# Kernel optimization log

Measured on AMD Instinct MI355X. Metric: run time of the kernel, lower is better.

## Reference

```python
import jax, jax.numpy as jnp
import numpy as np
import math

B, S, H = 8, 160, 768
DEP = 64
NH, DH = 12, H // 12
W_EDGE = 1.0
EPS = 1e-5


def setup_inputs() -> dict:
    key = jax.random.key(0)
    ks = jax.random.split(key, 16)
    sc_h = 1.0 / math.sqrt(H)
    sc_d = 1.0 / math.sqrt(DEP)
    return {
        "token_feature": jax.random.normal(ks[0], (B, S, H), jnp.float32),
        "edge_feature": jax.random.normal(ks[1], (B, S, S, DEP), jnp.float32),
        "dependency_masks": jax.random.randint(ks[2], (B, S, S), 0, 2, jnp.int32),
        "Wq": jax.random.normal(ks[3], (H, H), jnp.float32) * sc_h,
        "bq": jnp.zeros((H,), jnp.float32),
        "Wk": jax.random.normal(ks[4], (H, H), jnp.float32) * sc_h,
        "bk": jnp.zeros((H,), jnp.float32),
        "Wv": jax.random.normal(ks[5], (H, H), jnp.float32) * sc_h,
        "bv": jnp.zeros((H,), jnp.float32),
        "Wek": jax.random.normal(ks[6], (DEP, H), jnp.float32) * sc_d,
        "bek": jnp.zeros((H,), jnp.float32),
        "Wev": jax.random.normal(ks[7], (DEP, H), jnp.float32) * sc_d,
        "bev": jnp.zeros((H,), jnp.float32),
        "ln_g": jnp.ones((H,), jnp.float32),
        "ln_b": jnp.zeros((H,), jnp.float32),
    }


def _heads3(x):  # [B,S,H] -> [B,NH,S,DH]
    return x.reshape(B, S, NH, DH).transpose(0, 2, 1, 3)


def _heads4(x):  # [B,S,S,H] -> [B,NH,S,S,DH]
    return x.reshape(B, S, S, NH, DH).transpose(0, 3, 1, 2, 4)


def reference(token_feature, edge_feature, dependency_masks,
              Wq, bq, Wk, bk, Wv, bv, Wek, bek, Wev, bev, ln_g, ln_b):
    q = _heads3(token_feature @ Wq + bq)   # [B,NH,S,DH]
    k = _heads3(token_feature @ Wk + bk)
    v = _heads3(token_feature @ Wv + bv)
    ek = _heads4(edge_feature @ Wek + bek)  # [B,NH,S,S,DH]
    ev = _heads4(edge_feature @ Wev + bev)
    # key_ij = k_j + w*ek_ij ; scores_ij = q_i . key_ij / sqrt(dh)
    scores = (jnp.einsum('bhid,bhjd->bhij', q, k)
              + W_EDGE * jnp.einsum('bhid,bhijd->bhij', q, ek))
    scores = scores / math.sqrt(DH)
    mask = (dependency_masks[:, None, :, :] == 0)  # [B,1,S,S]
    scores = jnp.where(mask, jnp.float32(-10000.0), scores)
    probs = jax.nn.softmax(scores, axis=-1)  # dropout is identity in eval
    ctx = (jnp.einsum('bhij,bhjd->bhid', probs, v)
           + W_EDGE * jnp.einsum('bhij,bhijd->bhid', probs, ev))
    ctx = ctx.transpose(0, 2, 1, 3).reshape(B, S, H)
    x = token_feature + ctx
    mu = jnp.mean(x, axis=-1, keepdims=True)
    var = jnp.mean(jnp.square(x - mu), axis=-1, keepdims=True)
    return (x - mu) / jnp.sqrt(var + EPS) * ln_g + ln_b
```

## Files before the change

### kernel.cpp

```cpp
#include <hip/hip_runtime.h>
#include <hip/hip_bf16.h>
#include <math.h>

#define BB 8
#define SS 160
#define HH 768
#define DEPTH 64
#define NHEAD 12
#define DHEAD 64
#define BS (BB*SS)
#define SCROW (NHEAD*SS)

constexpr float EPS_C = 1e-5f;

typedef __attribute__((ext_vector_type(8))) short bf16x8;
typedef __attribute__((ext_vector_type(4))) float f32x4;

__device__ inline short f2bs(float x) {
    union { __hip_bfloat16 b; short s; } u;
    u.b = __float2bfloat16(x);
    return u.s;
}

__global__ __launch_bounds__(256) void transpose_cast_w(
    const float* __restrict__ Wq, const float* __restrict__ Wk,
    const float* __restrict__ Wv, __hip_bfloat16* __restrict__ WT)
{
    __shared__ float t[32][33];
    const float* W = (blockIdx.z == 0) ? Wq : (blockIdx.z == 1) ? Wk : Wv;
    __hip_bfloat16* o = WT + (size_t)blockIdx.z * HH * HH;
    int kt = blockIdx.x * 32, nt = blockIdx.y * 32;
    int tx = threadIdx.x & 31, ty = threadIdx.x >> 5;
#pragma unroll
    for (int r = 0; r < 32; r += 8)
        t[ty + r][tx] = W[(size_t)(kt + ty + r) * HH + nt + tx];
    __syncthreads();
#pragma unroll
    for (int r = 0; r < 32; r += 8)
        o[(size_t)(nt + ty + r) * HH + kt + tx] = __float2bfloat16(t[tx][ty + r]);
}

__global__ __launch_bounds__(256) void gemm_qkv(
    const float* __restrict__ X, const __hip_bfloat16* __restrict__ WT,
    const float* __restrict__ bq, const float* __restrict__ bk,
    const float* __restrict__ bv,
    __hip_bfloat16* __restrict__ qb, __hip_bfloat16* __restrict__ kb,
    __hip_bfloat16* __restrict__ vb)
{
    __shared__ int4 sA[4][128];
    __shared__ int4 sB[4][64];
    int m0 = blockIdx.x * 128, n0 = blockIdx.y * 64, mat = blockIdx.z;
    const short* W = (const short*)WT + (size_t)mat * HH * HH;
    const float* bias = (mat == 0) ? bq : (mat == 1) ? bk : bv;
    int tid = threadIdx.x, w = tid >> 6, l = tid & 63;
    int wm = (w >> 1) * 64, wn = (w & 1) * 32;
    int khalf = l >> 4, lc = l & 15;

    f32x4 acc[4][2];
#pragma unroll
    for (int i = 0; i < 4; i++)
#pragma unroll
        for (int j = 0; j < 2; j++) acc[i][j] = (f32x4){0.f, 0.f, 0.f, 0.f};

    for (int k0 = 0; k0 < HH; k0 += 32) {
        __syncthreads();
#pragma unroll
        for (int rr = 0; rr < 2; rr++) {
            const float* ap = X + (size_t)(m0 + l + rr * 64) * HH + k0 + w * 8;
            float4 x0 = *(const float4*)ap;
            float4 x1 = *(const float4*)(ap + 4);
            bf16x8 p;
            p[0]=f2bs(x0.x); p[1]=f2bs(x0.y); p[2]=f2bs(x0.z); p[3]=f2bs(x0.w);
            p[4]=f2bs(x1.x); p[5]=f2bs(x1.y); p[6]=f2bs(x1.z); p[7]=f2bs(x1.w);
            *(bf16x8*)&sA[w][l + rr * 64] = p;
        }
        sB[w][l] = *(const int4*)(W + (size_t)(n0 + l) * HH + k0 + w * 8);
        __syncthreads();
        bf16x8 b0 = *(const bf16x8*)&sB[khalf][wn + lc];
        bf16x8 b1 = *(const bf16x8*)&sB[khalf][wn + 16 + lc];
#pragma unroll
        for (int mi = 0; mi < 4; mi++) {
            bf16x8 a = *(const bf16x8*)&sA[khalf][wm + mi * 16 + lc];
            acc[mi][0] = __builtin_amdgcn_mfma_f32_16x16x32_bf16(a, b0, acc[mi][0], 0, 0, 0);
            acc[mi][1] = __builtin_amdgcn_mfma_f32_16x16x32_bf16(a, b1, acc[mi][1], 0, 0, 0);
        }
    }

    int rg = (l >> 4) * 4;
    __hip_bfloat16* outm = (mat == 0) ? qb : (mat == 1) ? kb : vb;
#pragma unroll
    for (int ni = 0; ni < 2; ni++) {
        int gcol = n0 + wn + ni * 16 + lc;
        float bv_ = bias[gcol];
#pragma unroll
        for (int mi = 0; mi < 4; mi++) {
            int grow = m0 + wm + mi * 16 + rg;
            f32x4 a = acc[mi][ni];
            __hip_bfloat16* o = outm + (size_t)grow * HH + gcol;
            o[0]      = __float2bfloat16(a.x + bv_);
            o[HH]     = __float2bfloat16(a.y + bv_);
            o[2 * HH] = __float2bfloat16(a.z + bv_);
            o[3 * HH] = __float2bfloat16(a.w + bv_);
        }
    }
}

__global__ __launch_bounds__(256) void scores_gemm(
    const __hip_bfloat16* __restrict__ qb, const __hip_bfloat16* __restrict__ kb,
    _Float16* __restrict__ sc)
{
    __shared__ int4 sQ[8][160];
    __shared__ int4 sK[8][160];
    int h = blockIdx.x, b = blockIdx.y;
    const short* Q = (const short*)qb + (size_t)b * SS * HH + h * DHEAD;
    const short* K = (const short*)kb + (size_t)b * SS * HH + h * DHEAD;
    int tid = threadIdx.x, w = tid >> 6, l = tid & 63;

    for (int idx = tid; idx < SS * 8; idx += 256) {
        int row = idx >> 3, ch = idx & 7;
        sQ[ch][row] = *(const int4*)(Q + (size_t)row * HH + ch * 8);
        sK[ch][row] = *(const int4*)(K + (size_t)row * HH + ch * 8);
    }
    __syncthreads();

    int wm = (w >> 1) * 80, wn = (w & 1) * 80;
    int khalf = l >> 4, lc = l & 15;
    f32x4 acc[5][5];
#pragma unroll
    for (int i = 0; i < 5; i++)
#pragma unroll
        for (int j = 0; j < 5; j++) acc[i][j] = (f32x4){0.f, 0.f, 0.f, 0.f};

#pragma unroll
    for (int s = 0; s < 2; s++) {
        int c = s * 4 + khalf;
        bf16x8 bf[5];
#pragma unroll
        for (int ni = 0; ni < 5; ni++)
            bf[ni] = *(const bf16x8*)&sK[c][wn + ni * 16 + lc];
#pragma unroll
        for (int mi = 0; mi < 5; mi++) {
            bf16x8 a = *(const bf16x8*)&sQ[c][wm + mi * 16 + lc];
#pragma unroll
            for (int ni = 0; ni < 5; ni++)
                acc[mi][ni] = __builtin_amdgcn_mfma_f32_16x16x32_bf16(a, bf[ni], acc[mi][ni], 0, 0, 0);
        }
    }

    int rg = (l >> 4) * 4;
    _Float16* base = sc + ((size_t)b * SS) * SCROW + (size_t)h * SS;
#pragma unroll
    for (int mi = 0; mi < 5; mi++) {
        int i0 = wm + mi * 16 + rg;
#pragma unroll
        for (int ni = 0; ni < 5; ni++) {
            int j = wn + ni * 16 + lc;
            f32x4 a = acc[mi][ni];
            base[(size_t)(i0 + 0) * SCROW + j] = (_Float16)(a.x * 0.125f);
            base[(size_t)(i0 + 1) * SCROW + j] = (_Float16)(a.y * 0.125f);
            base[(size_t)(i0 + 2) * SCROW + j] = (_Float16)(a.z * 0.125f);
            base[(size_t)(i0 + 3) * SCROW + j] = (_Float16)(a.w * 0.125f);
        }
    }
}

__global__ __launch_bounds__(256) void qek_slim(
    const __hip_bfloat16* __restrict__ qb, const float* __restrict__ Wek,
    __hip_bfloat16* __restrict__ qek)
{
    __shared__ short sW[8 * 65 * 8];
    int h = blockIdx.x, mg = blockIdx.y;
    int tid = threadIdx.x, w = tid >> 6, l = tid & 63;
    int lr = l & 15, kg = l >> 4;

    {
        int d = tid >> 2, q4 = tid & 3;
        const float* wp = Wek + (size_t)d * HH + h * DHEAD + q4 * 16;
        float4 w0 = *(const float4*)(wp);
        float4 w1 = *(const float4*)(wp + 4);
        float4 w2 = *(const float4*)(wp + 8);
        float4 w3 = *(const float4*)(wp + 12);
        bf16x8 p0, p1;
        p0[0]=f2bs(w0.x); p0[1]=f2bs(w0.y); p0[2]=f2bs(w0.z); p0[3]=f2bs(w0.w);
        p0[4]=f2bs(w1.x); p0[5]=f2bs(w1.y); p0[6]=f2bs(w1.z); p0[7]=f2bs(w1.w);
        p1[0]=f2bs(w2.x); p1[1]=f2bs(w2.y); p1[2]=f2bs(w2.z); p1[3]=f2bs(w2.w);
        p1[4]=f2bs(w3.x); p1[5]=f2bs(w3.y); p1[6]=f2bs(w3.z); p1[7]=f2bs(w3.w);
        *(bf16x8*)&sW[((q4 * 2) * 65 + d) * 8]     = p0;
        *(bf16x8*)&sW[((q4 * 2 + 1) * 65 + d) * 8] = p1;
    }
    __syncthreads();

    bf16x8 bfrag[2][4];
#pragma unroll
    for (int s = 0; s < 2; s++)
#pragma unroll
        for (int nt = 0; nt < 4; nt++)
            bfrag[s][nt] = *(const bf16x8*)&sW[((s * 4 + kg) * 65 + nt * 16 + lr) * 8];

    const short* Q = (const short*)qb;
    short* O = (short*)qek;
    int m0 = (mg * 4 + w) * 16;
    bf16x8 a0 = *(const bf16x8*)(Q + (size_t)(m0 + lr) * HH + h * DHEAD + kg * 8);
    bf16x8 a1 = *(const bf16x8*)(Q + (size_t)(m0 + lr) * HH + h * DHEAD + 32 + kg * 8);
#pragma unroll
    for (int nt = 0; nt < 4; nt++) {
        f32x4 acc = (f32x4){0.f, 0.f, 0.f, 0.f};
        acc = __builtin_amdgcn_mfma_f32_16x16x32_bf16(a0, bfrag[0][nt], acc, 0, 0, 0);
        acc = __builtin_amdgcn_mfma_f32_16x16x32_bf16(a1, bfrag[1][nt], acc, 0, 0, 0);
        int row0 = m0 + kg * 4;
#pragma unroll
        for (int r = 0; r < 4; r++)
            O[(size_t)(row0 + r) * HH + h * DHEAD + nt * 16 + lr] = f2bs(acc[r]);
    }
}

__global__ __launch_bounds__(256) void attn_kernel(
    const float* __restrict__ token, const float* __restrict__ edge,
    const int* __restrict__ mask,
    const __hip_bfloat16* __restrict__ q_ws, const _Float16* __restrict__ sc,
    const __hip_bfloat16* __restrict__ v_ws, const __hip_bfloat16* __restrict__ qek,
    const float* __restrict__ bek,
    const float* __restrict__ Wev, const float* __restrict__ bev,
    const float* __restrict__ ln_g, const float* __restrict__ ln_b,
    float* __restrict__ out)
{
    __shared__ float  s_ctx[HH];
    __shared__ float  s_scores[NHEAD][SS + 2];
    __shared__ float  s_pe[NHEAD][DEPTH];
    __shared__ float  s_x[HH];
    __shared__ float  s_qbek[NHEAD];
    __shared__ int    s_mask[SS];
    __shared__ float  s_red[8];

    int bi = blockIdx.x;
    int b  = bi / SS;
    int tid = threadIdx.x;
    int w = tid >> 6, l = tid & 63;
    int lr = l & 15, kg = l >> 4;

    if (tid < SS) s_mask[tid] = mask[(size_t)bi * SS + tid];

    {
        int hs = w * 3 + kg;
        float part = 0.f;
        if (hs < NHEAD) {
            const __hip_bfloat16* qp = q_ws + (size_t)bi * HH + hs * DHEAD + lr * 4;
            float4 bv4 = *(const float4*)(bek + hs * DHEAD + lr * 4);
            part = __bfloat162float(qp[0]) * bv4.x + __bfloat162float(qp[1]) * bv4.y
                 + __bfloat162float(qp[2]) * bv4.z + __bfloat162float(qp[3]) * bv4.w;
        }
        part += __shfl_xor(part, 1, 64);
        part += __shfl_xor(part, 2, 64);
        part += __shfl_xor(part, 4, 64);
        part += __shfl_xor(part, 8, 64);
        if (lr == 0 && hs < NHEAD) s_qbek[hs] = part;
    }
    __syncthreads();

    const float* scf = (const float*)(sc + (size_t)bi * SCROW);
    for (int idx = tid; idx < SCROW / 2; idx += 256) {
        int h = idx / (SS / 2), jp = idx - h * (SS / 2);
        union { float f; _Float16 e[2]; } u;
        u.f = scf[idx];
        int j = jp * 2;
        s_scores[h][j]     = s_mask[j]     ? ((float)u.e[0] + 0.125f * s_qbek[h]) : -10000.0f;
        s_scores[h][j + 1] = s_mask[j + 1] ? ((float)u.e[1] + 0.125f * s_qbek[h]) : -10000.0f;
    }
    __syncthreads();

    const float* e_row = edge + (size_t)bi * SS * DEPTH;
    {
        const short* QE = (const short*)qek + (size_t)bi * HH;
        bf16x8 qe0 = *(const bf16x8*)(QE + lr * DHEAD + kg * 8);
        bf16x8 qe1 = *(const bf16x8*)(QE + lr * DHEAD + 32 + kg * 8);
        for (int jt = w; jt < 10; jt += 4) {
            const float* ep = e_row + (size_t)(jt * 16 + lr) * DEPTH + kg * 8;
            float4 e0 = *(const float4*)(ep);
            float4 e1 = *(const float4*)(ep + 4);
            float4 e2 = *(const float4*)(ep + 32);
            float4 e3 = *(const float4*)(ep + 36);
            bf16x8 a0, a1;
            a0[0]=f2bs(e0.x); a0[1]=f2bs(e0.y); a0[2]=f2bs(e0.z); a0[3]=f2bs(e0.w);
            a0[4]=f2bs(e1.x); a0[5]=f2bs(e1.y); a0[6]=f2bs(e1.z); a0[7]=f2bs(e1.w);
            a1[0]=f2bs(e2.x); a1[1]=f2bs(e2.y); a1[2]=f2bs(e2.z); a1[3]=f2bs(e2.w);
            a1[4]=f2bs(e3.x); a1[5]=f2bs(e3.y); a1[6]=f2bs(e3.z); a1[7]=f2bs(e3.w);
            f32x4 acc = (f32x4){0.f, 0.f, 0.f, 0.f};
            acc = __builtin_amdgcn_mfma_f32_16x16x32_bf16(a0, qe0, acc, 0, 0, 0);
            acc = __builtin_amdgcn_mfma_f32_16x16x32_bf16(a1, qe1, acc, 0, 0, 0);
            if (lr < NHEAD) {
                int j0 = jt * 16 + kg * 4;
#pragma unroll
                for (int r = 0; r < 4; r++)
                    if (s_mask[j0 + r])
                        s_scores[lr][j0 + r] += 0.125f * acc[r];
            }
        }
    }
    __syncthreads();

    for (int h = w; h < NHEAD; h += 4) {
        float v0 = s_scores[h][l];
        float v1 = s_scores[h][l + 64];
        float v2 = (l < 32) ? s_scores[h][l + 128] : -INFINITY;
        float mx = fmaxf(v0, fmaxf(v1, v2));
#pragma unroll
        for (int mm = 32; mm >= 1; mm >>= 1) mx = fmaxf(mx, __shfl_xor(mx, mm, 64));
        float e0 = expf(v0 - mx), e1 = expf(v1 - mx);
        float e2 = (l < 32) ? expf(v2 - mx) : 0.f;
        float sm = e0 + e1 + e2;
#pragma unroll
        for (int mm = 32; mm >= 1; mm >>= 1) sm += __shfl_xor(sm, mm, 64);
        float inv = 1.0f / sm;
        s_scores[h][l]      = e0 * inv;
        s_scores[h][l + 64] = e1 * inv;
        if (l < 32) s_scores[h][l + 128] = e2 * inv;
    }
    __syncthreads();

    {
        int h0 = w * 3;
        float av0 = 0.f, av1 = 0.f, av2 = 0.f;
        float pe0 = 0.f, pe1 = 0.f, pe2 = 0.f;
        const __hip_bfloat16* vbp = v_ws + (size_t)b * SS * HH + h0 * DHEAD + l;
        const float* er = e_row + l;
#pragma unroll 2
        for (int j0 = 0; j0 < SS; j0 += 2) {
            float2 p0 = *(const float2*)(&s_scores[h0][j0]);
            float2 p1 = *(const float2*)(&s_scores[h0 + 1][j0]);
            float2 p2 = *(const float2*)(&s_scores[h0 + 2][j0]);
            const __hip_bfloat16* vp = vbp + (size_t)j0 * HH;
            av0 += p0.x * __bfloat162float(vp[0])
                 + p0.y * __bfloat162float(vp[HH]);
            av1 += p1.x * __bfloat162float(vp[DHEAD])
                 + p1.y * __bfloat162float(vp[HH + DHEAD]);
            av2 += p2.x * __bfloat162float(vp[2 * DHEAD])
                 + p2.y * __bfloat162float(vp[HH + 2 * DHEAD]);
            float ev0 = er[(size_t)j0 * DEPTH];
            float ev1 = er[(size_t)(j0 + 1) * DEPTH];
            pe0 += p0.x * ev0 + p0.y * ev1;
            pe1 += p1.x * ev0 + p1.y * ev1;
            pe2 += p2.x * ev0 + p2.y * ev1;
        }
        s_pe[h0][l]     = pe0;
        s_pe[h0 + 1][l] = pe1;
        s_pe[h0 + 2][l] = pe2;
        s_ctx[h0 * DHEAD + l]       = av0;
        s_ctx[(h0 + 1) * DHEAD + l] = av1;
        s_ctx[(h0 + 2) * DHEAD + l] = av2;
    }
    __syncthreads();

    for (int mdx = tid; mdx < HH; mdx += 256) {
        int h = mdx >> 6;
        const float* pep = &s_pe[h][0];
        float sum = 0.f;
#pragma unroll
        for (int d = 0; d < DEPTH; d++) sum += pep[d] * Wev[(size_t)d * HH + mdx];
        float ctx = s_ctx[mdx] + (sum + bev[mdx]);
        s_x[mdx] = token[(size_t)bi * HH + mdx] + ctx;
    }
    __syncthreads();

    float lsum = 0.f, lsq = 0.f;
    for (int c = tid; c < HH; c += 256) {
        float x = s_x[c];
        lsum += x; lsq += x * x;
    }
#pragma unroll
    for (int mm = 32; mm >= 1; mm >>= 1) {
        lsum += __shfl_xor(lsum, mm, 64);
        lsq  += __shfl_xor(lsq,  mm, 64);
    }
    if (l == 0) { s_red[w] = lsum; s_red[4 + w] = lsq; }
    __syncthreads();
    float tsum = s_red[0] + s_red[1] + s_red[2] + s_red[3];
    float tsq  = s_red[4] + s_red[5] + s_red[6] + s_red[7];
    float mu  = tsum / HH;
    float var = tsq / HH - mu * mu;
    float rstd = rsqrtf(var + EPS_C);
    for (int c = tid; c < HH; c += 256)
        out[(size_t)bi * HH + c] = (s_x[c] - mu) * rstd * ln_g[c] + ln_b[c];
}

extern "C" void kernel_launch(void* const* d_in, const int* in_sizes, int n_in,
                              void* d_out, int out_size, void* d_ws, size_t ws_size,
                              hipStream_t stream) {
    const float* token = (const float*)d_in[0];
    const float* edge  = (const float*)d_in[1];
    const int*   mask  = (const int*)d_in[2];
    const float* Wq = (const float*)d_in[3];  const float* bq = (const float*)d_in[4];
    const float* Wk = (const float*)d_in[5];  const float* bk = (const float*)d_in[6];
    const float* Wv = (const float*)d_in[7];  const float* bv = (const float*)d_in[8];
    const float* Wek = (const float*)d_in[9];  const float* bek = (const float*)d_in[10];
    const float* Wev = (const float*)d_in[11]; const float* bev = (const float*)d_in[12];
    const float* ln_g = (const float*)d_in[13]; const float* ln_b = (const float*)d_in[14];
    float* out = (float*)d_out;

    __hip_bfloat16* qb = (__hip_bfloat16*)d_ws;
    __hip_bfloat16* kb = qb + (size_t)BS * HH;
    __hip_bfloat16* vb = kb + (size_t)BS * HH;
    __hip_bfloat16* WT = vb + (size_t)BS * HH;
    _Float16*       sc = (_Float16*)WT;
    __hip_bfloat16* qek = kb;

    transpose_cast_w<<<dim3(24, 24, 3), 256, 0, stream>>>(Wq, Wk, Wv, WT);
    gemm_qkv<<<dim3(BS / 128, HH / 64, 3), 256, 0, stream>>>(
        token, WT, bq, bk, bv, qb, kb, vb);
    scores_gemm<<<dim3(NHEAD, BB), 256, 0, stream>>>(qb, kb, sc);
    qek_slim<<<dim3(NHEAD, 20), 256, 0, stream>>>(qb, Wek, qek);
    attn_kernel<<<BS, 256, 0, stream>>>(token, edge, mask, qb, sc, vb, qek,
                                        bek, Wev, bev, ln_g, ln_b, out);
}
```

Measured before the change: 113.1 us.

## Store V transposed and split edge-score MFMA into a separate kernel

The QKV GEMM now writes V in a per-batch transposed layout so the attention kernel can load eight consecutive keys per lane with one vector load instead of scalar strided bf16 loads. The edge-key score contribution (edge x qek via MFMA) moves out of the attention kernel into a new escore_add2 kernel that adds into the fp16 score buffer in global memory, shortening attn_kernel and removing one barrier. The trade-off is an extra launch, an extra read-modify-write pass over the score buffer with fp16 rounding of the combined score, and strided transposed stores in the GEMM epilogue. The edge tensor is also read twice, once per kernel.

Result: slower. 200.2 us (+77.1%).

```diff
diff --git a/kernel.cpp b/kernel.cpp
--- a/kernel.cpp
+++ b/kernel.cpp
@@ -21,6 +21,11 @@
     u.b = __float2bfloat16(x);
     return u.s;
 }
+__device__ inline float bs2f(short s) {
+    union { short s; __hip_bfloat16 b; } u;
+    u.s = s;
+    return __bfloat162float(u.b);
+}
 
 __global__ __launch_bounds__(256) void transpose_cast_w(
     const float* __restrict__ Wq, const float* __restrict__ Wk,
@@ -45,7 +50,7 @@
     const float* __restrict__ bq, const float* __restrict__ bk,
     const float* __restrict__ bv,
     __hip_bfloat16* __restrict__ qb, __hip_bfloat16* __restrict__ kb,
-    __hip_bfloat16* __restrict__ vb)
+    __hip_bfloat16* __restrict__ vTb)
 {
     __shared__ int4 sA[4][128];
     __shared__ int4 sB[4][64];
@@ -87,7 +92,6 @@
     }
 
     int rg = (l >> 4) * 4;
-    __hip_bfloat16* outm = (mat == 0) ? qb : (mat == 1) ? kb : vb;
 #pragma unroll
     for (int ni = 0; ni < 2; ni++) {
         int gcol = n0 + wn + ni * 16 + lc;
@@ -96,11 +100,20 @@
         for (int mi = 0; mi < 4; mi++) {
             int grow = m0 + wm + mi * 16 + rg;
             f32x4 a = acc[mi][ni];
-            __hip_bfloat16* o = outm + (size_t)grow * HH + gcol;
-            o[0]      = __float2bfloat16(a.x + bv_);
-            o[HH]     = __float2bfloat16(a.y + bv_);
-            o[2 * HH] = __float2bfloat16(a.z + bv_);
-            o[3 * HH] = __float2bfloat16(a.w + bv_);
+            if (mat == 2) {
+                int bb = grow / SS; int i0 = grow - bb * SS;
+                __hip_bfloat16* dst = vTb + ((size_t)bb * HH + gcol) * SS + i0;
+                dst[0] = __float2bfloat16(a.x + bv_);
+                dst[1] = __float2bfloat16(a.y + bv_);
+                dst[2] = __float2bfloat16(a.z + bv_);
+                dst[3] = __float2bfloat16(a.w + bv_);
+            } else {
+                __hip_bfloat16* o = ((mat == 0) ? qb : kb) + (size_t)grow * HH + gcol;
+                o[0]      = __float2bfloat16(a.x + bv_);
+                o[HH]     = __float2bfloat16(a.y + bv_);
+                o[2 * HH] = __float2bfloat16(a.z + bv_);
+                o[3 * HH] = __float2bfloat16(a.w + bv_);
+            }
         }
     }
 }
@@ -214,11 +227,53 @@
     }
 }
 
+__global__ __launch_bounds__(256) void escore_add2(
+    const float* __restrict__ edge, const __hip_bfloat16* __restrict__ qek,
+    _Float16* __restrict__ sc)
+{
+    int task = blockIdx.x * 4 + (threadIdx.x >> 6);
+    int l = threadIdx.x & 63;
+    int bi = task / 5, seg = task - (task / 5) * 5;
+    int lr = l & 15, kg = l >> 4;
+
+    const short* QE = (const short*)qek + (size_t)bi * HH;
+    bf16x8 qe0 = *(const bf16x8*)(QE + lr * DHEAD + kg * 8);
+    bf16x8 qe1 = *(const bf16x8*)(QE + lr * DHEAD + 32 + kg * 8);
+
+    const float* E = edge + (size_t)bi * SS * DEPTH;
+    _Float16* srow = sc + (size_t)bi * SCROW;
+
+#pragma unroll
+    for (int t = 0; t < 2; t++) {
+        int jt = seg * 2 + t;
+        const float* ep = E + (size_t)(jt * 16 + lr) * DEPTH + kg * 8;
+        float4 e0 = *(const float4*)(ep);
+        float4 e1 = *(const float4*)(ep + 4);
+        float4 e2 = *(const float4*)(ep + 32);
+        float4 e3 = *(const float4*)(ep + 36);
+        bf16x8 a0, a1;
+        a0[0]=f2bs(e0.x); a0[1]=f2bs(e0.y); a0[2]=f2bs(e0.z); a0[3]=f2bs(e0.w);
+        a0[4]=f2bs(e1.x); a0[5]=f2bs(e1.y); a0[6]=f2bs(e1.z); a0[7]=f2bs(e1.w);
+        a1[0]=f2bs(e2.x); a1[1]=f2bs(e2.y); a1[2]=f2bs(e2.z); a1[3]=f2bs(e2.w);
+        a1[4]=f2bs(e3.x); a1[5]=f2bs(e3.y); a1[6]=f2bs(e3.z); a1[7]=f2bs(e3.w);
+        f32x4 acc = (f32x4){0.f, 0.f, 0.f, 0.f};
+        acc = __builtin_amdgcn_mfma_f32_16x16x32_bf16(a0, qe0, acc, 0, 0, 0);
+        acc = __builtin_amdgcn_mfma_f32_16x16x32_bf16(a1, qe1, acc, 0, 0, 0);
+        if (lr < NHEAD) {
+            int j0 = jt * 16 + kg * 4;
+            _Float16* p = srow + (size_t)lr * SS + j0;
+#pragma unroll
+            for (int r = 0; r < 4; r++)
+                p[r] = (_Float16)((float)p[r] + 0.125f * acc[r]);
+        }
+    }
+}
+
 __global__ __launch_bounds__(256) void attn_kernel(
     const float* __restrict__ token, const float* __restrict__ edge,
     const int* __restrict__ mask,
     const __hip_bfloat16* __restrict__ q_ws, const _Float16* __restrict__ sc,
-    const __hip_bfloat16* __restrict__ v_ws, const __hip_bfloat16* __restrict__ qek,
+    const __hip_bfloat16* __restrict__ vT,
     const float* __restrict__ bek,
     const float* __restrict__ Wev, const float* __restrict__ bev,
     const float* __restrict__ ln_g, const float* __restrict__ ln_b,
@@ -268,36 +323,6 @@
     }
     __syncthreads();
 
-    const float* e_row = edge + (size_t)bi * SS * DEPTH;
-    {
-        const short* QE = (const short*)qek + (size_t)bi * HH;
-        bf16x8 qe0 = *(const bf16x8*)(QE + lr * DHEAD + kg * 8);
-        bf16x8 qe1 = *(const bf16x8*)(QE + lr * DHEAD + 32 + kg * 8);
-        for (int jt = w; jt < 10; jt += 4) {
-            const float* ep = e_row + (size_t)(jt * 16 + lr) * DEPTH + kg * 8;
-            float4 e0 = *(const float4*)(ep);
-            float4 e1 = *(const float4*)(ep + 4);
-            float4 e2 = *(const float4*)(ep + 32);
-            float4 e3 = *(const float4*)(ep + 36);
-            bf16x8 a0, a1;
-            a0[0]=f2bs(e0.x); a0[1]=f2bs(e0.y); a0[2]=f2bs(e0.z); a0[3]=f2bs(e0.w);
-            a0[4]=f2bs(e1.x); a0[5]=f2bs(e1.y); a0[6]=f2bs(e1.z); a0[7]=f2bs(e1.w);
-            a1[0]=f2bs(e2.x); a1[1]=f2bs(e2.y); a1[2]=f2bs(e2.z); a1[3]=f2bs(e2.w);
-            a1[4]=f2bs(e3.x); a1[5]=f2bs(e3.y); a1[6]=f2bs(e3.z); a1[7]=f2bs(e3.w);
-            f32x4 acc = (f32x4){0.f, 0.f, 0.f, 0.f};
-            acc = __builtin_amdgcn_mfma_f32_16x16x32_bf16(a0, qe0, acc, 0, 0, 0);
-            acc = __builtin_amdgcn_mfma_f32_16x16x32_bf16(a1, qe1, acc, 0, 0, 0);
-            if (lr < NHEAD) {
-                int j0 = jt * 16 + kg * 4;
-#pragma unroll
-                for (int r = 0; r < 4; r++)
-                    if (s_mask[j0 + r])
-                        s_scores[lr][j0 + r] += 0.125f * acc[r];
-            }
-        }
-    }
-    __syncthreads();
-
     for (int h = w; h < NHEAD; h += 4) {
         float v0 = s_scores[h][l];
         float v1 = s_scores[h][l + 64];
@@ -317,29 +342,33 @@
     }
     __syncthreads();
 
+    const float* e_row = edge + (size_t)bi * SS * DEPTH;
     {
         int h0 = w * 3;
         float av0 = 0.f, av1 = 0.f, av2 = 0.f;
         float pe0 = 0.f, pe1 = 0.f, pe2 = 0.f;
-        const __hip_bfloat16* vbp = v_ws + (size_t)b * SS * HH + h0 * DHEAD + l;
+        const __hip_bfloat16* vt0 = vT + ((size_t)b * HH + h0 * DHEAD + l) * SS;
+        const __hip_bfloat16* vt1 = vt0 + (size_t)DHEAD * SS;
+        const __hip_bfloat16* vt2 = vt1 + (size_t)DHEAD * SS;
         const float* er = e_row + l;
-#pragma unroll 2
-        for (int j0 = 0; j0 < SS; j0 += 2) {
-            float2 p0 = *(const float2*)(&s_scores[h0][j0]);
-            float2 p1 = *(const float2*)(&s_scores[h0 + 1][j0]);
-            float2 p2 = *(const float2*)(&s_scores[h0 + 2][j0]);
-            const __hip_bfloat16* vp = vbp + (size_t)j0 * HH;
-            av0 += p0.x * __bfloat162float(vp[0])
-                 + p0.y * __bfloat162float(vp[HH]);
-            av1 += p1.x * __bfloat162float(vp[DHEAD])
-                 + p1.y * __bfloat162float(vp[HH + DHEAD]);
-            av2 += p2.x * __bfloat162float(vp[2 * DHEAD])
-                 + p2.y * __bfloat162float(vp[HH + 2 * DHEAD]);
-            float ev0 = er[(size_t)j0 * DEPTH];
-            float ev1 = er[(size_t)(j0 + 1) * DEPTH];
-            pe0 += p0.x * ev0 + p0.y * ev1;
-            pe1 += p1.x * ev0 + p1.y * ev1;
-            pe2 += p2.x * ev0 + p2.y * ev1;
+        for (int j0 = 0; j0 < SS; j0 += 8) {
+            bf16x8 v0 = *(const bf16x8*)(vt0 + j0);
+            bf16x8 v1 = *(const bf16x8*)(vt1 + j0);
+            bf16x8 v2 = *(const bf16x8*)(vt2 + j0);
+#pragma unroll
+            for (int r = 0; r < 8; r += 2) {
+                float2 p0 = *(const float2*)(&s_scores[h0][j0 + r]);
+                float2 p1 = *(const float2*)(&s_scores[h0 + 1][j0 + r]);
+                float2 p2 = *(const float2*)(&s_scores[h0 + 2][j0 + r]);
+                float ev0 = er[(size_t)(j0 + r) * DEPTH];
+                float ev1 = er[(size_t)(j0 + r + 1) * DEPTH];
+                av0 += p0.x * bs2f(v0[r]) + p0.y * bs2f(v0[r + 1]);
+                av1 += p1.x * bs2f(v1[r]) + p1.y * bs2f(v1[r + 1]);
+                av2 += p2.x * bs2f(v2[r]) + p2.y * bs2f(v2[r + 1]);
+                pe0 += p0.x * ev0 + p0.y * ev1;
+                pe1 += p1.x * ev0 + p1.y * ev1;
+                pe2 += p2.x * ev0 + p2.y * ev1;
+            }
         }
         s_pe[h0][l]     = pe0;
         s_pe[h0 + 1][l] = pe1;
@@ -398,16 +427,17 @@
 
     __hip_bfloat16* qb = (__hip_bfloat16*)d_ws;
     __hip_bfloat16* kb = qb + (size_t)BS * HH;
-    __hip_bfloat16* vb = kb + (size_t)BS * HH;
-    __hip_bfloat16* WT = vb + (size_t)BS * HH;
+    __hip_bfloat16* vT = kb + (size_t)BS * HH;
+    __hip_bfloat16* WT = vT + (size_t)BS * HH;
     _Float16*       sc = (_Float16*)WT;
     __hip_bfloat16* qek = kb;
 
     transpose_cast_w<<<dim3(24, 24, 3), 256, 0, stream>>>(Wq, Wk, Wv, WT);
     gemm_qkv<<<dim3(BS / 128, HH / 64, 3), 256, 0, stream>>>(
-        token, WT, bq, bk, bv, qb, kb, vb);
+        token, WT, bq, bk, bv, qb, kb, vT);
     scores_gemm<<<dim3(NHEAD, BB), 256, 0, stream>>>(qb, kb, sc);
     qek_slim<<<dim3(NHEAD, 20), 256, 0, stream>>>(qb, Wek, qek);
-    attn_kernel<<<BS, 256, 0, stream>>>(token, edge, mask, qb, sc, vb, qek,
+    escore_add2<<<1600, 256, 0, stream>>>(edge, qek, sc);
+    attn_kernel<<<BS, 256, 0, stream>>>(token, edge, mask, qb, sc, vT,
                                         bek, Wev, bev, ln_g, ln_b, out);
 }
```
